# Performance work log

Measured on AMD Instinct MI355X. Metric: run time of the kernel, lower is better.

Reference implementation:

```python
import jax, jax.numpy as jnp
import numpy as np

DIM = 2048
HEADS = 16
HEAD_DIM = DIM // HEADS


def setup_inputs() -> dict:
    key = jax.random.key(0)
    ks = jax.random.split(key, 9)
    B, S = 1, 4096
    X = jax.random.normal(ks[0], (B, S, DIM), dtype=jnp.float32)
    sc = 1.0 / np.sqrt(DIM)
    Wq = jax.random.normal(ks[1], (DIM, DIM), dtype=jnp.float32) * sc
    bq = jax.random.normal(ks[2], (DIM,), dtype=jnp.float32) * 0.01
    Wk = jax.random.normal(ks[3], (DIM, DIM), dtype=jnp.float32) * sc
    bk = jax.random.normal(ks[4], (DIM,), dtype=jnp.float32) * 0.01
    Wv = jax.random.normal(ks[5], (DIM, DIM), dtype=jnp.float32) * sc
    bv = jax.random.normal(ks[6], (DIM,), dtype=jnp.float32) * 0.01
    Wo = jax.random.normal(ks[7], (DIM, DIM), dtype=jnp.float32) * sc
    bo = jax.random.normal(ks[8], (DIM,), dtype=jnp.float32) * 0.01
    return {"X": X, "Wq": Wq, "bq": bq, "Wk": Wk, "bk": bk,
            "Wv": Wv, "bv": bv, "Wo": Wo, "bo": bo, "is_causal": 1}


def reference(X, Wq, bq, Wk, bk, Wv, bv, Wo, bo, is_causal):
    B, S, _ = X.shape
    # torch nn.Linear: y = x @ W^T + b
    Q = (X @ Wq.T + bq).reshape(B, S, HEADS, HEAD_DIM).transpose(0, 2, 1, 3)
    K = (X @ Wk.T + bk).reshape(B, S, HEADS, HEAD_DIM).transpose(0, 2, 1, 3)
    V = (X @ Wv.T + bv).reshape(B, S, HEADS, HEAD_DIM).transpose(0, 2, 1, 3)
    scores = jnp.einsum('bhqd,bhkd->bhqk', Q, K) / np.sqrt(HEAD_DIM)  # [B,H,S,S]
    if is_causal:
        causal = jnp.tril(jnp.ones((S, S), dtype=bool))
        scores = jnp.where(causal, scores, -jnp.inf)
    attn = jax.nn.softmax(scores, axis=-1)
    # dropout_rate = 0 (eval) -> identity
    Out = jnp.einsum('bhqk,bhkd->bhqd', attn, V)
    Out = Out.transpose(0, 2, 1, 3).reshape(B, S, DIM)
    return Out @ Wo.T + bo
```

## Files before the change

### kernel.cpp

```cpp
#include <hip/hip_runtime.h>
#include <hip/hip_bf16.h>

typedef unsigned short u16;
typedef __attribute__((ext_vector_type(8))) short short8;
typedef __attribute__((ext_vector_type(4))) short short4v;
typedef __attribute__((ext_vector_type(4))) float floatx4;

constexpr int SEQ = 4096;
constexpr int DM  = 2048;
constexpr int NH  = 16;
constexpr int HD  = 128;

__device__ inline u16 f2b(float f) {
    __hip_bfloat16 h = __float2bfloat16(f);
    return *reinterpret_cast<u16*>(&h);
}
__device__ inline float b2f(u16 u) {
    __hip_bfloat16 h = *reinterpret_cast<__hip_bfloat16*>(&u);
    return __bfloat162float(h);
}

__device__ __forceinline__ void async_copy16(const u16* g, u16* lds_base) {
    __builtin_amdgcn_global_load_lds(
        (const __attribute__((address_space(1))) unsigned int*)g,
        (__attribute__((address_space(3))) unsigned int*)lds_base,
        16, 0, 0);
}

template<int N> __device__ __forceinline__ void wait_vm() {
    if constexpr (N == 0) asm volatile("s_waitcnt vmcnt(0)" ::: "memory");
    else if constexpr (N == 2) asm volatile("s_waitcnt vmcnt(2)" ::: "memory");
    else if constexpr (N == 3) asm volatile("s_waitcnt vmcnt(3)" ::: "memory");
    else if constexpr (N == 4) asm volatile("s_waitcnt vmcnt(4)" ::: "memory");
}
template<int N> __device__ __forceinline__ void wait_lgkm() {
    if constexpr (N == 0) asm volatile("s_waitcnt lgkmcnt(0)" ::: "memory");
    else if constexpr (N == 4) asm volatile("s_waitcnt lgkmcnt(4)" ::: "memory");
    else if constexpr (N == 8) asm volatile("s_waitcnt lgkmcnt(8)" ::: "memory");
    else if constexpr (N == 10) asm volatile("s_waitcnt lgkmcnt(10)" ::: "memory");
    else if constexpr (N == 12) asm volatile("s_waitcnt lgkmcnt(12)" ::: "memory");
}

__global__ void detect_dtype(const u16* __restrict__ X, int* __restrict__ flag) {
    __shared__ int cnt;
    if (threadIdx.x == 0) cnt = 0;
    __syncthreads();
    int local = 0;
    for (int i = threadIdx.x; i < 4096; i += 256) {
        int e = (X[i] >> 7) & 0xFF;
        if (e >= 0x3C && e <= 0x8D) local++;
    }
    atomicAdd(&cnt, local);
    __syncthreads();
    if (threadIdx.x == 0) *flag = (cnt >= 3890) ? 1 : 0;
}

struct ConvArgs {
    const void* src[9];
    unsigned long long dstoff[9];
    int n[9];
};
__global__ void convert_all(ConvArgs a, u16* __restrict__ base,
                            const int* __restrict__ flag) {
    const int t = blockIdx.y;
    const int n = a.n[t];
    const int i = (blockIdx.x * blockDim.x + threadIdx.x) * 8;
    if (i >= n) return;
    u16* out = base + a.dstoff[t];
    if (*flag) {
        *(short8*)&out[i] = *(const short8*)&((const u16*)a.src[t])[i];
    } else {
        const float* p = (const float*)a.src[t];
        u16 tmp[8];
#pragma unroll
        for (int j = 0; j < 8; j++) tmp[j] = f2b(p[i + j]);
        *(short8*)&out[i] = *(const short8*)tmp;
    }
}

template<int NF>
__device__ __forceinline__ void gemm_core(
    const u16* __restrict__ A, const u16* __restrict__ W,
    int m0, int n0, floatx4 (&acc)[8][NF])
{
    __shared__ __align__(16) u16 As[2][16384];
    __shared__ __align__(16) u16 Bs[2][NF * 4096];
    constexpr int K  = DM;
    constexpr int NT = K / 64;
    constexpr int B1N = (NF + 1) / 2;

    const int tid  = threadIdx.x;
    const int lane = tid & 63;
    const int w    = tid >> 6;
    const int qm   = lane & 15;
    const int quad = lane >> 4;
    const int wm   = (w >> 2) * 128;
    const int wn   = (w & 3) * (NF * 16);

    const int srow = tid >> 3;
    const int scol = ((tid & 7) ^ (srow & 7)) * 8;

    const int fo0 = (quad ^ (qm & 7)) * 8;
    const int fo1 = fo0 ^ 32;

    const u16* Ag = A + (size_t)(m0 + srow) * K + scol;
    const u16* Wg = W + (size_t)(n0 + srow) * K + scol;

#define STG_A_ALL(par, k0) {                                                    \
    async_copy16(Ag + (size_t)0 * 64 * K + (k0), &As[par][0 * 4096 + w * 512]); \
    async_copy16(Ag + (size_t)1 * 64 * K + (k0), &As[par][1 * 4096 + w * 512]); \
    async_copy16(Ag + (size_t)2 * 64 * K + (k0), &As[par][2 * 4096 + w * 512]); \
    async_copy16(Ag + (size_t)3 * 64 * K + (k0), &As[par][3 * 4096 + w * 512]); }
#define STG_B_SLOT(s, par, k0)                                                  \
    async_copy16(Wg + (size_t)(s) * 64 * K + (k0), &Bs[par][(s) * 4096 + w * 512]);

#define RD_AQ(dst, Abase, q) {                                                  \
    dst[0][0] = *(const short8*)&Abase[(wm + (2*(q)) * 16 + qm) * 64 + fo0];    \
    dst[0][1] = *(const short8*)&Abase[(wm + (2*(q)) * 16 + qm) * 64 + fo1];    \
    dst[1][0] = *(const short8*)&Abase[(wm + (2*(q)+1) * 16 + qm) * 64 + fo0];  \
    dst[1][1] = *(const short8*)&Abase[(wm + (2*(q)+1) * 16 + qm) * 64 + fo1]; }

#define RD_B(dst, Bbase) {                                                      \
    _Pragma("unroll")                                                           \
    for (int nt = 0; nt < NF; ++nt) {                                           \
        dst[nt][0] = *(const short8*)&Bbase[(wn + nt * 16 + qm) * 64 + fo0];    \
        dst[nt][1] = *(const short8*)&Bbase[(wn + nt * 16 + qm) * 64 + fo1];    \
    } }

#define MFMA_Q(q, aR, bR) {                                                     \
    __builtin_amdgcn_s_setprio(1);                                              \
    _Pragma("unroll")                                                           \
    for (int nt = 0; nt < NF; ++nt) {                                           \
        acc[2*(q)][nt]   = __builtin_amdgcn_mfma_f32_16x16x32_bf16(aR[0][0], bR[nt][0], acc[2*(q)][nt],   0, 0, 0); \
        acc[2*(q)][nt]   = __builtin_amdgcn_mfma_f32_16x16x32_bf16(aR[0][1], bR[nt][1], acc[2*(q)][nt],   0, 0, 0); \
        acc[2*(q)+1][nt] = __builtin_amdgcn_mfma_f32_16x16x32_bf16(aR[1][0], bR[nt][0], acc[2*(q)+1][nt], 0, 0, 0); \
        acc[2*(q)+1][nt] = __builtin_amdgcn_mfma_f32_16x16x32_bf16(aR[1][1], bR[nt][1], acc[2*(q)+1][nt], 0, 0, 0); \
    }                                                                           \
    __builtin_amdgcn_s_setprio(0); }

#define TILE_BODY(T, BCUR, BNXT) {                                              \
    const int P = (T) & 1;                                                      \
    const u16* Ac = As[P];                                                      \
    const int kA = ((T) + 1) * 64, kB = ((T) + 2) * 64;                         \
    const bool m1 = (T) + 1 < NT, m2 = (T) + 2 < NT;                            \
                                     \
    RD_AQ(aY, Ac, 1);                                                           \
    if (m1) STG_A_ALL(P ^ 1, kA);                                               \
    __builtin_amdgcn_s_barrier();                                               \
    wait_lgkm<4>();                                                             \
    __builtin_amdgcn_sched_barrier(0);                                          \
    MFMA_Q(0, aX, BCUR);                                                        \
    __builtin_amdgcn_s_barrier();                                               \
                         \
    RD_AQ(aX, Ac, 2);                                                           \
    if (m2) { _Pragma("unroll")                                                 \
              for (int s = 0; s < B1N; ++s) STG_B_SLOT(s, P, kB); }             \
    __builtin_amdgcn_s_barrier();                                               \
    wait_lgkm<4>();                                                             \
    __builtin_amdgcn_sched_barrier(0);                                          \
    MFMA_Q(1, aY, BCUR);                                                        \
    __builtin_amdgcn_s_barrier();                                               \
                 \
    RD_AQ(aY, Ac, 3);                                                           \
    if (m2) { _Pragma("unroll")                                                 \
              for (int s = B1N; s < NF; ++s) STG_B_SLOT(s, P, kB); }            \
    __builtin_amdgcn_s_barrier();                                               \
    wait_lgkm<4>();                                                             \
    __builtin_amdgcn_sched_barrier(0);                                          \
    MFMA_Q(2, aX, BCUR);                                                        \
    if (m2) wait_vm<NF>(); else wait_vm<0>();                                   \
    __builtin_amdgcn_s_barrier();                                               \
           \
    if (m1) { RD_B(BNXT, Bs[P ^ 1]); RD_AQ(aX, As[P ^ 1], 0); }                 \
    __builtin_amdgcn_s_barrier();                                               \
    if (m1) wait_lgkm<2 * NF + 4>(); else wait_lgkm<0>();                       \
    __builtin_amdgcn_sched_barrier(0);                                          \
    MFMA_Q(3, aY, BCUR);                                                        \
    __builtin_amdgcn_s_barrier(); }

#pragma unroll
    for (int i = 0; i < 8; ++i)
#pragma unroll
        for (int j = 0; j < NF; ++j) acc[i][j] = floatx4{0.f, 0.f, 0.f, 0.f};

    short8 Bu[NF][2], Bv[NF][2];
    short8 aX[2][2], aY[2][2];

#pragma unroll
    for (int s = 0; s < NF; ++s) STG_B_SLOT(s, 0, 0);
    STG_A_ALL(0, 0);
#pragma unroll
    for (int s = 0; s < NF; ++s) STG_B_SLOT(s, 1, 64);
    wait_vm<NF>();
    __builtin_amdgcn_s_barrier();
    RD_B(Bu, Bs[0]);
    RD_AQ(aX, As[0], 0);

    for (int t2 = 0; t2 < NT; t2 += 2) {
        TILE_BODY(t2,     Bu, Bv);
        TILE_BODY(t2 + 1, Bv, Bu);
    }
#undef STG_A_ALL
#undef STG_B_SLOT
#undef RD_AQ
#undef RD_B
#undef MFMA_Q
#undef TILE_BODY
}

__launch_bounds__(512, 2)
__global__ void gemm_qkv(const u16* __restrict__ A, const u16* __restrict__ W,
                         const u16* __restrict__ bias,
                         u16* __restrict__ Qb, u16* __restrict__ Kb,
                         u16* __restrict__ VtG) {
    const int m0 = blockIdx.y * 256;
    const int n0 = blockIdx.x * 192;
    floatx4 acc[8][3];
    gemm_core<3>(A, W, m0, n0, acc);

    const int tid  = threadIdx.x;
    const int lane = tid & 63;
    const int w    = tid >> 6;
    const int qm   = lane & 15;
    const int quad = lane >> 4;
    const int wm   = (w >> 2) * 128;
    const int wn   = (w & 3) * 48;

#pragma unroll
    for (int nt = 0; nt < 3; ++nt) {
        const int gc0  = n0 + wn + nt * 16;
        const int buf  = gc0 >> 11;
        const int gcol = gc0 + qm;
        const int col  = gcol & 2047;
        const float bv = b2f(bias[gcol]);
        if (buf < 2) {
            u16* Y = (buf == 0) ? Qb : Kb;
#pragma unroll
            for (int mt = 0; mt < 8; ++mt) {
                const int rbase = m0 + wm + mt * 16 + quad * 4;
#pragma unroll
                for (int r = 0; r < 4; ++r)
                    Y[(size_t)(rbase + r) * DM + col] = f2b(acc[mt][nt][r] + bv);
            }
        } else {
#pragma unroll
            for (int mt = 0; mt < 8; ++mt) {
                const int rbase = m0 + wm + mt * 16 + quad * 4;
                u16 tmp[4];
#pragma unroll
                for (int r = 0; r < 4; ++r)
                    tmp[r] = f2b(acc[mt][nt][r] + bv);
                *(short4v*)&VtG[(size_t)col * SEQ + rbase] = *(const short4v*)tmp;
            }
        }
    }
}

__launch_bounds__(512, 2)
__global__ void gemm_out(const u16* __restrict__ A, const u16* __restrict__ W,
                         const u16* __restrict__ bias, void* __restrict__ out,
                         const int* __restrict__ flag) {
    const int m0 = blockIdx.y * 256;
    const int n0 = blockIdx.x * 128;
    floatx4 acc[8][2];
    gemm_core<2>(A, W, m0, n0, acc);

    const int tid  = threadIdx.x;
    const int lane = tid & 63;
    const int w    = tid >> 6;
    const int qm   = lane & 15;
    const int quad = lane >> 4;
    const int wm   = (w >> 2) * 128;
    const int wn   = (w & 3) * 32;
    const int N    = DM;

    const int f = *flag;
#pragma unroll
    for (int nt = 0; nt < 2; ++nt) {
        const int col = n0 + wn + nt * 16 + qm;
        const float bv = b2f(bias[col]);
#pragma unroll
        for (int mt = 0; mt < 8; ++mt) {
            const int rbase = m0 + wm + mt * 16 + quad * 4;
#pragma unroll
            for (int r = 0; r < 4; ++r) {
                const float v = acc[mt][nt][r] + bv;
                if (f) ((u16*)out)[(size_t)(rbase + r) * N + col] = f2b(v);
                else   ((float*)out)[(size_t)(rbase + r) * N + col] = v;
            }
        }
    }
}

__launch_bounds__(512)
__global__ void attn_kernel(const u16* __restrict__ Q, const u16* __restrict__ K,
                            const u16* __restrict__ Vt, u16* __restrict__ O,
                            const int* __restrict__ is_causal_p) {
    __shared__ __align__(16) u16 Ks[64][136];
    __shared__ __align__(16) u16 Vts[128][72];
    __shared__ __align__(16) u16 Pb[8][16][72];

    const int tid  = threadIdx.x;
    const int lane = tid & 63;
    const int w    = tid >> 6;
    const int qm   = lane & 15;
    const int quad = lane >> 4;
    const int xt   = ((blockIdx.y >> 3) & 1) ? (gridDim.x - 1 - blockIdx.x)
                                             : blockIdx.x;
    const int q0   = xt * 128;
    const int h    = blockIdx.y;
    const int causal = *is_causal_p;
    const float scale = 0.08838834764831845f;
    const float SHIFT = 16.0f;

    short8 qf[4];
    {
        const u16* qptr = Q + (size_t)(q0 + w * 16 + qm) * DM + h * HD;
#pragma unroll
        for (int kc = 0; kc < 4; kc++)
            qf[kc] = *(const short8*)&qptr[kc * 32 + quad * 8];
    }

    floatx4 o[8];
#pragma unroll
    for (int dt = 0; dt < 8; dt++) o[dt] = floatx4{0.f, 0.f, 0.f, 0.f};
    float l_part[4] = {0.f, 0.f, 0.f, 0.f};

    const int jend = causal ? (q0 + 128) : SEQ;

    const int kr0 = tid >> 4;
    const int kc8 = (tid & 15) * 8;
    const int vd0 = tid >> 3;
    const int vc8 = (tid & 7) * 8;

    short8 kreg[2], vreg[2];
#pragma unroll
    for (int p = 0; p < 2; p++) {
        kreg[p] = *(const short8*)&K[(size_t)(kr0 + p * 32) * DM + h * HD + kc8];
        vreg[p] = *(const short8*)&Vt[(size_t)(h * HD + vd0 + p * 64) * SEQ + vc8];
    }

    for (int j0 = 0; j0 < jend; j0 += 64) {
#pragma unroll
        for (int p = 0; p < 2; p++) {
            *(short8*)&Ks[kr0 + p * 32][kc8] = kreg[p];
            *(short8*)&Vts[vd0 + p * 64][vc8] = vreg[p];
        }
        __syncthreads();

        const int jn = (j0 + 64 < jend) ? j0 + 64 : 0;
#pragma unroll
        for (int p = 0; p < 2; p++) {
            kreg[p] = *(const short8*)&K[(size_t)(jn + kr0 + p * 32) * DM + h * HD + kc8];
            vreg[p] = *(const short8*)&Vt[(size_t)(h * HD + vd0 + p * 64) * SEQ + jn + vc8];
        }

        floatx4 s[4];
#pragma unroll
        for (int nt = 0; nt < 4; nt++) s[nt] = floatx4{0.f, 0.f, 0.f, 0.f};
        __builtin_amdgcn_s_setprio(1);
#pragma unroll
        for (int kc = 0; kc < 4; kc++)
#pragma unroll
            for (int nt = 0; nt < 4; nt++) {
                short8 b = *(const short8*)&Ks[nt * 16 + qm][kc * 32 + quad * 8];
                s[nt] = __builtin_amdgcn_mfma_f32_16x16x32_bf16(qf[kc], b, s[nt], 0, 0, 0);
            }
        __builtin_amdgcn_s_setprio(0);

        const bool mask = causal && (j0 + 64 > q0 + w * 16);
#pragma unroll
        for (int r = 0; r < 4; r++) {
            const int qg = q0 + w * 16 + quad * 4 + r;
#pragma unroll
            for (int nt = 0; nt < 4; nt++) {
                float v = fmaf(s[nt][r], scale, -SHIFT);
                if (mask && (j0 + nt * 16 + qm > qg)) v = -1e30f;
                const float p = __expf(v);
                l_part[r] += p;
                Pb[w][quad * 4 + r][nt * 16 + qm] = f2b(p);
            }
        }
        asm volatile("s_waitcnt lgkmcnt(0)" ::: "memory");

        __builtin_amdgcn_s_setprio(1);
#pragma unroll
        for (int kc = 0; kc < 2; kc++) {
            short8 pf = *(const short8*)&Pb[w][qm][kc * 32 + quad * 8];
#pragma unroll
            for (int dt = 0; dt < 8; dt++) {
                short8 b = *(const short8*)&Vts[dt * 16 + qm][kc * 32 + quad * 8];
                o[dt] = __builtin_amdgcn_mfma_f32_16x16x32_bf16(pf, b, o[dt], 0, 0, 0);
            }
        }
        __builtin_amdgcn_s_setprio(0);
        __syncthreads();
    }

#pragma unroll
    for (int r = 0; r < 4; r++) {
        float l = l_part[r];
#pragma unroll
        for (int off = 8; off >= 1; off >>= 1)
            l += __shfl_xor(l, off, 64);
        const float inv = 1.0f / l;
        const int qg = q0 + w * 16 + quad * 4 + r;
#pragma unroll
        for (int dt = 0; dt < 8; dt++) {
            const int d = h * HD + dt * 16 + qm;
            O[(size_t)qg * DM + d] = f2b(o[dt][r] * inv);
        }
    }
}

extern "C" void kernel_launch(void* const* d_in, const int* in_sizes, int n_in,
                              void* d_out, int out_size, void* d_ws, size_t ws_size,
                              hipStream_t stream) {
    const int* isc = (const int*)d_in[9];

    int* flag = (int*)d_ws;
    u16* base = (u16*)((char*)d_ws + 256);

    const int NX = SEQ * DM;
    const int NW = DM * DM;
    const int NB = DM;

    unsigned long long off = 0;
    const unsigned long long oXc   = off; off += NX;
    const unsigned long long oWall = off; off += 3ull * NW;
    const unsigned long long oWo   = off; off += NW;
    const unsigned long long oBall = off; off += 3ull * NB;
    const unsigned long long oBo   = off; off += NB;
    const unsigned long long oQ    = off; off += NX;
    const unsigned long long oK    = off; off += NX;
    const unsigned long long oVt   = off; off += NX;
    const unsigned long long oA    = off; off += NX;

    detect_dtype<<<1, 256, 0, stream>>>((const u16*)d_in[0], flag);

    ConvArgs ca;
    const unsigned long long dsts[9] = {oXc, oWall, oBall, oWall + NW, oBall + NB,
                                        oWall + 2ull * NW, oBall + 2ull * NB, oWo, oBo};
    for (int i = 0; i < 9; i++) {
        ca.src[i] = d_in[i];
        ca.dstoff[i] = dsts[i];
        ca.n[i] = in_sizes[i];
    }
    convert_all<<<dim3(NX / 8 / 256, 9), 256, 0, stream>>>(ca, base, flag);

    gemm_qkv<<<dim3(3 * DM / 192, SEQ / 256), 512, 0, stream>>>(
        base + oXc, base + oWall, base + oBall,
        base + oQ, base + oK, base + oVt);

    attn_kernel<<<dim3(SEQ / 128, NH), 512, 0, stream>>>(
        base + oQ, base + oK, base + oVt, base + oA, isc);

    gemm_out<<<dim3(DM / 128, SEQ / 256), 512, 0, stream>>>(
        base + oA, base + oWo, base + oBo, d_out, flag);
}
```

Before: 441.0 us.

## Restructure attention to 4 waves with 32 query rows each and swizzled grid

The attention kernel moves from 8 waves of 16 query rows to 4 waves of 32 rows, so each K fragment read from LDS feeds two MFMAs and LDS traffic per FLOP drops. The P tile is staged in LDS as fp32 and converted to bf16 at read time. The softmax switches to exp2 with a prescaled log2e factor and a larger shift. A 1D grid with an XCD-aware swizzle replaces the 2D grid and keeps the reversed-order load balancing. The trade-off is more registers per thread (launch bounds 256,2) and doubled P staging bytes, plus a fixed shift with no running max that risks overflow for large scores.

```diff
diff --git a/kernel.cpp b/kernel.cpp
--- a/kernel.cpp
+++ b/kernel.cpp
@@ -143,7 +143,6 @@
     const u16* Ac = As[P];                                                      \
     const int kA = ((T) + 1) * 64, kB = ((T) + 2) * 64;                         \
     const bool m1 = (T) + 1 < NT, m2 = (T) + 2 < NT;                            \
-                                     \
     RD_AQ(aY, Ac, 1);                                                           \
     if (m1) STG_A_ALL(P ^ 1, kA);                                               \
     __builtin_amdgcn_s_barrier();                                               \
@@ -151,7 +150,6 @@
     __builtin_amdgcn_sched_barrier(0);                                          \
     MFMA_Q(0, aX, BCUR);                                                        \
     __builtin_amdgcn_s_barrier();                                               \
-                         \
     RD_AQ(aX, Ac, 2);                                                           \
     if (m2) { _Pragma("unroll")                                                 \
               for (int s = 0; s < B1N; ++s) STG_B_SLOT(s, P, kB); }             \
@@ -160,7 +158,6 @@
     __builtin_amdgcn_sched_barrier(0);                                          \
     MFMA_Q(1, aY, BCUR);                                                        \
     __builtin_amdgcn_s_barrier();                                               \
-                 \
     RD_AQ(aY, Ac, 3);                                                           \
     if (m2) { _Pragma("unroll")                                                 \
               for (int s = B1N; s < NF; ++s) STG_B_SLOT(s, P, kB); }            \
@@ -170,7 +167,6 @@
     MFMA_Q(2, aX, BCUR);                                                        \
     if (m2) wait_vm<NF>(); else wait_vm<0>();                                   \
     __builtin_amdgcn_s_barrier();                                               \
-           \
     if (m1) { RD_B(BNXT, Bs[P ^ 1]); RD_AQ(aX, As[P ^ 1], 0); }                 \
     __builtin_amdgcn_s_barrier();                                               \
     if (m1) wait_lgkm<2 * NF + 4>(); else wait_lgkm<0>();                       \
@@ -292,39 +288,45 @@
     }
 }
 
-__launch_bounds__(512)
+__launch_bounds__(256, 2)
 __global__ void attn_kernel(const u16* __restrict__ Q, const u16* __restrict__ K,
                             const u16* __restrict__ Vt, u16* __restrict__ O,
                             const int* __restrict__ is_causal_p) {
     __shared__ __align__(16) u16 Ks[64][136];
     __shared__ __align__(16) u16 Vts[128][72];
-    __shared__ __align__(16) u16 Pb[8][16][72];
+    __shared__ __align__(16) float Pbf[4][32][68];
 
     const int tid  = threadIdx.x;
     const int lane = tid & 63;
     const int w    = tid >> 6;
     const int qm   = lane & 15;
     const int quad = lane >> 4;
-    const int xt   = ((blockIdx.y >> 3) & 1) ? (gridDim.x - 1 - blockIdx.x)
-                                             : blockIdx.x;
-    const int q0   = xt * 128;
-    const int h    = blockIdx.y;
+
+    const int dd  = blockIdx.x;
+    const int swz = (dd & 7) * 64 + (dd >> 3);
+    const int h   = swz >> 5;
+    const int xr  = swz & 31;
+    const int xt  = (h & 1) ? (31 - xr) : xr;
+    const int q0  = xt * 128;
     const int causal = *is_causal_p;
-    const float scale = 0.08838834764831845f;
-    const float SHIFT = 16.0f;
-
-    short8 qf[4];
-    {
-        const u16* qptr = Q + (size_t)(q0 + w * 16 + qm) * DM + h * HD;
+    const float scl2 = 0.08838834764831845f * 1.4426950408889634f;
+    const float SH2  = 23.0f;
+
+    short8 qf[2][4];
+#pragma unroll
+    for (int qs = 0; qs < 2; qs++) {
+        const u16* qptr = Q + (size_t)(q0 + w * 32 + qs * 16 + qm) * DM + h * HD;
 #pragma unroll
         for (int kc = 0; kc < 4; kc++)
-            qf[kc] = *(const short8*)&qptr[kc * 32 + quad * 8];
-    }
-
-    floatx4 o[8];
-#pragma unroll
-    for (int dt = 0; dt < 8; dt++) o[dt] = floatx4{0.f, 0.f, 0.f, 0.f};
-    float l_part[4] = {0.f, 0.f, 0.f, 0.f};
+            qf[qs][kc] = *(const short8*)&qptr[kc * 32 + quad * 8];
+    }
+
+    floatx4 o[2][8];
+#pragma unroll
+    for (int qs = 0; qs < 2; qs++)
+#pragma unroll
+        for (int dt = 0; dt < 8; dt++) o[qs][dt] = floatx4{0.f, 0.f, 0.f, 0.f};
+    float l_part[2][4] = {{0.f, 0.f, 0.f, 0.f}, {0.f, 0.f, 0.f, 0.f}};
 
     const int jend = causal ? (q0 + 128) : SEQ;
 
@@ -333,84 +335,100 @@
     const int vd0 = tid >> 3;
     const int vc8 = (tid & 7) * 8;
 
-    short8 kreg[2], vreg[2];
-#pragma unroll
-    for (int p = 0; p < 2; p++) {
-        kreg[p] = *(const short8*)&K[(size_t)(kr0 + p * 32) * DM + h * HD + kc8];
-        vreg[p] = *(const short8*)&Vt[(size_t)(h * HD + vd0 + p * 64) * SEQ + vc8];
+    short8 kreg[4], vreg[4];
+#pragma unroll
+    for (int p = 0; p < 4; p++) {
+        kreg[p] = *(const short8*)&K[(size_t)(kr0 + p * 16) * DM + h * HD + kc8];
+        vreg[p] = *(const short8*)&Vt[(size_t)(h * HD + vd0 + p * 32) * SEQ + vc8];
     }
 
     for (int j0 = 0; j0 < jend; j0 += 64) {
 #pragma unroll
-        for (int p = 0; p < 2; p++) {
-            *(short8*)&Ks[kr0 + p * 32][kc8] = kreg[p];
-            *(short8*)&Vts[vd0 + p * 64][vc8] = vreg[p];
+        for (int p = 0; p < 4; p++) {
+            *(short8*)&Ks[kr0 + p * 16][kc8] = kreg[p];
+            *(short8*)&Vts[vd0 + p * 32][vc8] = vreg[p];
         }
         __syncthreads();
 
         const int jn = (j0 + 64 < jend) ? j0 + 64 : 0;
 #pragma unroll
-        for (int p = 0; p < 2; p++) {
-            kreg[p] = *(const short8*)&K[(size_t)(jn + kr0 + p * 32) * DM + h * HD + kc8];
-            vreg[p] = *(const short8*)&Vt[(size_t)(h * HD + vd0 + p * 64) * SEQ + jn + vc8];
-        }
-
-        floatx4 s[4];
-#pragma unroll
-        for (int nt = 0; nt < 4; nt++) s[nt] = floatx4{0.f, 0.f, 0.f, 0.f};
+        for (int p = 0; p < 4; p++) {
+            kreg[p] = *(const short8*)&K[(size_t)(jn + kr0 + p * 16) * DM + h * HD + kc8];
+            vreg[p] = *(const short8*)&Vt[(size_t)(h * HD + vd0 + p * 32) * SEQ + jn + vc8];
+        }
+
+        floatx4 s[2][4];
+#pragma unroll
+        for (int qs = 0; qs < 2; qs++)
+#pragma unroll
+            for (int nt = 0; nt < 4; nt++) s[qs][nt] = floatx4{0.f, 0.f, 0.f, 0.f};
         __builtin_amdgcn_s_setprio(1);
 #pragma unroll
         for (int kc = 0; kc < 4; kc++)
 #pragma unroll
             for (int nt = 0; nt < 4; nt++) {
                 short8 b = *(const short8*)&Ks[nt * 16 + qm][kc * 32 + quad * 8];
-                s[nt] = __builtin_amdgcn_mfma_f32_16x16x32_bf16(qf[kc], b, s[nt], 0, 0, 0);
+                s[0][nt] = __builtin_amdgcn_mfma_f32_16x16x32_bf16(qf[0][kc], b, s[0][nt], 0, 0, 0);
+                s[1][nt] = __builtin_amdgcn_mfma_f32_16x16x32_bf16(qf[1][kc], b, s[1][nt], 0, 0, 0);
             }
         __builtin_amdgcn_s_setprio(0);
 
-        const bool mask = causal && (j0 + 64 > q0 + w * 16);
-#pragma unroll
-        for (int r = 0; r < 4; r++) {
-            const int qg = q0 + w * 16 + quad * 4 + r;
-#pragma unroll
-            for (int nt = 0; nt < 4; nt++) {
-                float v = fmaf(s[nt][r], scale, -SHIFT);
-                if (mask && (j0 + nt * 16 + qm > qg)) v = -1e30f;
-                const float p = __expf(v);
-                l_part[r] += p;
-                Pb[w][quad * 4 + r][nt * 16 + qm] = f2b(p);
+#pragma unroll
+        for (int qs = 0; qs < 2; qs++) {
+            const int rowb = w * 32 + qs * 16;
+            const bool mask = causal && (j0 + 64 > q0 + rowb);
+#pragma unroll
+            for (int r = 0; r < 4; r++) {
+                const int qg = q0 + rowb + quad * 4 + r;
+#pragma unroll
+                for (int nt = 0; nt < 4; nt++) {
+                    float v = fmaf(s[qs][nt][r], scl2, -SH2);
+                    if (mask && (j0 + nt * 16 + qm > qg)) v = -1e30f;
+                    const float p = exp2f(v);
+                    l_part[qs][r] += p;
+                    Pbf[w][qs * 16 + quad * 4 + r][nt * 16 + qm] = p;
+                }
             }
         }
         asm volatile("s_waitcnt lgkmcnt(0)" ::: "memory");
 
         __builtin_amdgcn_s_setprio(1);
 #pragma unroll
-        for (int kc = 0; kc < 2; kc++) {
-            short8 pf = *(const short8*)&Pb[w][qm][kc * 32 + quad * 8];
-#pragma unroll
-            for (int dt = 0; dt < 8; dt++) {
-                short8 b = *(const short8*)&Vts[dt * 16 + qm][kc * 32 + quad * 8];
-                o[dt] = __builtin_amdgcn_mfma_f32_16x16x32_bf16(pf, b, o[dt], 0, 0, 0);
-            }
-        }
+        for (int qs = 0; qs < 2; qs++)
+#pragma unroll
+            for (int kc = 0; kc < 2; kc++) {
+                const float* prow = &Pbf[w][qs * 16 + qm][kc * 32 + quad * 8];
+                floatx4 p0 = *(const floatx4*)prow;
+                floatx4 p1 = *(const floatx4*)(prow + 4);
+                short8 pf;
+#pragma unroll
+                for (int e = 0; e < 4; e++) { pf[e] = (short)f2b(p0[e]); pf[e + 4] = (short)f2b(p1[e]); }
+#pragma unroll
+                for (int dt = 0; dt < 8; dt++) {
+                    short8 b = *(const short8*)&Vts[dt * 16 + qm][kc * 32 + quad * 8];
+                    o[qs][dt] = __builtin_amdgcn_mfma_f32_16x16x32_bf16(pf, b, o[qs][dt], 0, 0, 0);
+                }
+            }
         __builtin_amdgcn_s_setprio(0);
         __syncthreads();
     }
 
 #pragma unroll
-    for (int r = 0; r < 4; r++) {
-        float l = l_part[r];
-#pragma unroll
-        for (int off = 8; off >= 1; off >>= 1)
-            l += __shfl_xor(l, off, 64);
-        const float inv = 1.0f / l;
-        const int qg = q0 + w * 16 + quad * 4 + r;
-#pragma unroll
-        for (int dt = 0; dt < 8; dt++) {
-            const int d = h * HD + dt * 16 + qm;
-            O[(size_t)qg * DM + d] = f2b(o[dt][r] * inv);
-        }
-    }
+    for (int qs = 0; qs < 2; qs++)
+#pragma unroll
+        for (int r = 0; r < 4; r++) {
+            float l = l_part[qs][r];
+#pragma unroll
+            for (int off = 8; off >= 1; off >>= 1)
+                l += __shfl_xor(l, off, 64);
+            const float inv = 1.0f / l;
+            const int qg = q0 + w * 32 + qs * 16 + quad * 4 + r;
+#pragma unroll
+            for (int dt = 0; dt < 8; dt++) {
+                const int d = h * HD + dt * 16 + qm;
+                O[(size_t)qg * DM + d] = f2b(o[qs][dt][r] * inv);
+            }
+        }
 }
 
 extern "C" void kernel_launch(void* const* d_in, const int* in_sizes, int n_in,
@@ -452,7 +470,7 @@
         base + oXc, base + oWall, base + oBall,
         base + oQ, base + oK, base + oVt);
 
-    attn_kernel<<<dim3(SEQ / 128, NH), 512, 0, stream>>>(
+    attn_kernel<<<dim3(512), 256, 0, stream>>>(
         base + oQ, base + oK, base + oVt, base + oA, isc);
 
     gemm_out<<<dim3(DM / 128, SEQ / 256), 512, 0, stream>>>(
```

Result: slower. 463.5 us (+5.1%).

## Swizzle attention LDS tiles, remap grid, use exp2 and fp32 P buffer

Applied to the files above, without the earlier changes.

In the attention kernel, the padded K/V LDS arrays are replaced by unpadded ones with an XOR column swizzle to avoid bank conflicts. The 2D grid becomes a 1D grid with a block index swizzle that spreads heads and query tiles across dispatch order. Softmax now uses exp2 with a pre-multiplied log2e scale. P is stored as fp32 in LDS and converted to bf16 when read, which trades more LDS traffic for fewer scattered 16-bit stores. Launch bounds add a min-blocks hint of 4.

```diff
diff --git a/kernel.cpp b/kernel.cpp
--- a/kernel.cpp
+++ b/kernel.cpp
@@ -143,7 +143,6 @@
     const u16* Ac = As[P];                                                      \
     const int kA = ((T) + 1) * 64, kB = ((T) + 2) * 64;                         \
     const bool m1 = (T) + 1 < NT, m2 = (T) + 2 < NT;                            \
-                                     \
     RD_AQ(aY, Ac, 1);                                                           \
     if (m1) STG_A_ALL(P ^ 1, kA);                                               \
     __builtin_amdgcn_s_barrier();                                               \
@@ -151,7 +150,6 @@
     __builtin_amdgcn_sched_barrier(0);                                          \
     MFMA_Q(0, aX, BCUR);                                                        \
     __builtin_amdgcn_s_barrier();                                               \
-                         \
     RD_AQ(aX, Ac, 2);                                                           \
     if (m2) { _Pragma("unroll")                                                 \
               for (int s = 0; s < B1N; ++s) STG_B_SLOT(s, P, kB); }             \
@@ -160,7 +158,6 @@
     __builtin_amdgcn_sched_barrier(0);                                          \
     MFMA_Q(1, aY, BCUR);                                                        \
     __builtin_amdgcn_s_barrier();                                               \
-                 \
     RD_AQ(aY, Ac, 3);                                                           \
     if (m2) { _Pragma("unroll")                                                 \
               for (int s = B1N; s < NF; ++s) STG_B_SLOT(s, P, kB); }            \
@@ -170,7 +167,6 @@
     MFMA_Q(2, aX, BCUR);                                                        \
     if (m2) wait_vm<NF>(); else wait_vm<0>();                                   \
     __builtin_amdgcn_s_barrier();                                               \
-           \
     if (m1) { RD_B(BNXT, Bs[P ^ 1]); RD_AQ(aX, As[P ^ 1], 0); }                 \
     __builtin_amdgcn_s_barrier();                                               \
     if (m1) wait_lgkm<2 * NF + 4>(); else wait_lgkm<0>();                       \
@@ -292,26 +288,29 @@
     }
 }
 
-__launch_bounds__(512)
+__launch_bounds__(512, 4)
 __global__ void attn_kernel(const u16* __restrict__ Q, const u16* __restrict__ K,
                             const u16* __restrict__ Vt, u16* __restrict__ O,
                             const int* __restrict__ is_causal_p) {
-    __shared__ __align__(16) u16 Ks[64][136];
-    __shared__ __align__(16) u16 Vts[128][72];
-    __shared__ __align__(16) u16 Pb[8][16][72];
+    __shared__ __align__(16) u16 Ks[64][128];
+    __shared__ __align__(16) u16 Vts[128][64];
+    __shared__ __align__(16) float Pbf[8][16][68];
 
     const int tid  = threadIdx.x;
     const int lane = tid & 63;
     const int w    = tid >> 6;
     const int qm   = lane & 15;
     const int quad = lane >> 4;
-    const int xt   = ((blockIdx.y >> 3) & 1) ? (gridDim.x - 1 - blockIdx.x)
-                                             : blockIdx.x;
-    const int q0   = xt * 128;
-    const int h    = blockIdx.y;
+
+    const int dd  = blockIdx.x;
+    const int swz = (dd & 7) * 64 + (dd >> 3);
+    const int h   = swz >> 5;
+    const int xr  = swz & 31;
+    const int xt  = (h & 1) ? (31 - xr) : xr;
+    const int q0  = xt * 128;
     const int causal = *is_causal_p;
-    const float scale = 0.08838834764831845f;
-    const float SHIFT = 16.0f;
+    const float scl2 = 0.08838834764831845f * 1.4426950408889634f;
+    const float SH2  = 23.0f;
 
     short8 qf[4];
     {
@@ -329,30 +328,38 @@
     const int jend = causal ? (q0 + 128) : SEQ;
 
     const int kr0 = tid >> 4;
-    const int kc8 = (tid & 15) * 8;
+    const int gk  = tid & 15;
+    const int kcs = (gk ^ (kr0 & 7)) * 8;
+    const int kcg = gk * 8;
     const int vd0 = tid >> 3;
-    const int vc8 = (tid & 7) * 8;
+    const int gv  = tid & 7;
+    const int vcs = (gv ^ (vd0 & 7)) * 8;
+    const int vcg = gv * 8;
+
+    int fk[4];
+#pragma unroll
+    for (int kc = 0; kc < 4; kc++) fk[kc] = ((kc * 4 + quad) ^ (qm & 7)) * 8;
 
     short8 kreg[2], vreg[2];
 #pragma unroll
     for (int p = 0; p < 2; p++) {
-        kreg[p] = *(const short8*)&K[(size_t)(kr0 + p * 32) * DM + h * HD + kc8];
-        vreg[p] = *(const short8*)&Vt[(size_t)(h * HD + vd0 + p * 64) * SEQ + vc8];
+        kreg[p] = *(const short8*)&K[(size_t)(kr0 + p * 32) * DM + h * HD + kcg];
+        vreg[p] = *(const short8*)&Vt[(size_t)(h * HD + vd0 + p * 64) * SEQ + vcg];
     }
 
     for (int j0 = 0; j0 < jend; j0 += 64) {
 #pragma unroll
         for (int p = 0; p < 2; p++) {
-            *(short8*)&Ks[kr0 + p * 32][kc8] = kreg[p];
-            *(short8*)&Vts[vd0 + p * 64][vc8] = vreg[p];
+            *(short8*)&Ks[kr0 + p * 32][kcs] = kreg[p];
+            *(short8*)&Vts[vd0 + p * 64][vcs] = vreg[p];
         }
         __syncthreads();
 
         const int jn = (j0 + 64 < jend) ? j0 + 64 : 0;
 #pragma unroll
         for (int p = 0; p < 2; p++) {
-            kreg[p] = *(const short8*)&K[(size_t)(jn + kr0 + p * 32) * DM + h * HD + kc8];
-            vreg[p] = *(const short8*)&Vt[(size_t)(h * HD + vd0 + p * 64) * SEQ + jn + vc8];
+            kreg[p] = *(const short8*)&K[(size_t)(jn + kr0 + p * 32) * DM + h * HD + kcg];
+            vreg[p] = *(const short8*)&Vt[(size_t)(h * HD + vd0 + p * 64) * SEQ + jn + vcg];
         }
 
         floatx4 s[4];
@@ -363,7 +370,7 @@
         for (int kc = 0; kc < 4; kc++)
 #pragma unroll
             for (int nt = 0; nt < 4; nt++) {
-                short8 b = *(const short8*)&Ks[nt * 16 + qm][kc * 32 + quad * 8];
+                short8 b = *(const short8*)&Ks[nt * 16 + qm][fk[kc]];
                 s[nt] = __builtin_amdgcn_mfma_f32_16x16x32_bf16(qf[kc], b, s[nt], 0, 0, 0);
             }
         __builtin_amdgcn_s_setprio(0);
@@ -374,11 +381,11 @@
             const int qg = q0 + w * 16 + quad * 4 + r;
 #pragma unroll
             for (int nt = 0; nt < 4; nt++) {
-                float v = fmaf(s[nt][r], scale, -SHIFT);
+                float v = fmaf(s[nt][r], scl2, -SH2);
                 if (mask && (j0 + nt * 16 + qm > qg)) v = -1e30f;
-                const float p = __expf(v);
+                const float p = exp2f(v);
                 l_part[r] += p;
-                Pb[w][quad * 4 + r][nt * 16 + qm] = f2b(p);
+                Pbf[w][quad * 4 + r][nt * 16 + qm] = p;
             }
         }
         asm volatile("s_waitcnt lgkmcnt(0)" ::: "memory");
@@ -386,10 +393,15 @@
         __builtin_amdgcn_s_setprio(1);
 #pragma unroll
         for (int kc = 0; kc < 2; kc++) {
-            short8 pf = *(const short8*)&Pb[w][qm][kc * 32 + quad * 8];
+            const float* prow = &Pbf[w][qm][kc * 32 + quad * 8];
+            floatx4 p0 = *(const floatx4*)prow;
+            floatx4 p1 = *(const floatx4*)(prow + 4);
+            short8 pf;
+#pragma unroll
+            for (int e = 0; e < 4; e++) { pf[e] = (short)f2b(p0[e]); pf[e + 4] = (short)f2b(p1[e]); }
 #pragma unroll
             for (int dt = 0; dt < 8; dt++) {
-                short8 b = *(const short8*)&Vts[dt * 16 + qm][kc * 32 + quad * 8];
+                short8 b = *(const short8*)&Vts[dt * 16 + qm][fk[kc]];
                 o[dt] = __builtin_amdgcn_mfma_f32_16x16x32_bf16(pf, b, o[dt], 0, 0, 0);
             }
         }
@@ -452,7 +464,7 @@
         base + oXc, base + oWall, base + oBall,
         base + oQ, base + oK, base + oVt);
 
-    attn_kernel<<<dim3(SEQ / 128, NH), 512, 0, stream>>>(
+    attn_kernel<<<dim3(512), 512, 0, stream>>>(
         base + oQ, base + oK, base + oVt, base + oA, isc);
 
     gemm_out<<<dim3(DM / 128, SEQ / 256), 512, 0, stream>>>(
```

Result: slower. 454.8 us (+3.1%).
